# Kernel optimization log

Hardware: AMD Instinct MI355X
Metric: run time of the kernel (lower is better)

The kernel has to match this reference:

```python
import jax, jax.numpy as jnp
import numpy as np

D_MODEL = 256
LATENT = 64
OBJ = 32
OUT_DIM = LATENT + OBJ  # 96
STEPS = 50
BETA_START = 1e-4
BETA_END = 0.02
LN_EPS = 1e-5


def _gru_layer(x, w_ih, w_hh, b_ih, b_hh):
    # x: [B, T, din]; weights in torch layout: [3*d, din], [3*d, d]
    B = x.shape[0]
    d = w_hh.shape[1]

    def step(h, xt):
        gi = xt @ w_ih.T + b_ih
        gh = h @ w_hh.T + b_hh
        i_r, i_z, i_n = jnp.split(gi, 3, axis=-1)
        h_r, h_z, h_n = jnp.split(gh, 3, axis=-1)
        r = jax.nn.sigmoid(i_r + h_r)
        z = jax.nn.sigmoid(i_z + h_z)
        n = jnp.tanh(i_n + r * h_n)
        h_new = (1.0 - z) * n + z * h
        return h_new, h_new

    h0 = jnp.zeros((B, d), x.dtype)
    _, ys = jax.lax.scan(step, h0, jnp.swapaxes(x, 0, 1))
    return jnp.swapaxes(ys, 0, 1)


def setup_inputs() -> dict:
    key = jax.random.key(0)
    ks = jax.random.split(key, 24)
    B, T = 8, 512
    D, IN = D_MODEL, OUT_DIM
    s = 0.02
    inp = {
        "z_seq": jax.random.normal(ks[0], (B, T, LATENT), jnp.float32),
        "o_seq": jax.random.normal(ks[1], (B, T, OBJ), jnp.float32),
        "in_proj_w": jax.random.normal(ks[2], (D, IN), jnp.float32) * s,
        "in_proj_b": jnp.zeros((D,), jnp.float32),
        "gru_wih0": jax.random.normal(ks[3], (3 * D, D), jnp.float32) * s,
        "gru_whh0": jax.random.normal(ks[4], (3 * D, D), jnp.float32) * s,
        "gru_bih0": jnp.zeros((3 * D,), jnp.float32),
        "gru_bhh0": jnp.zeros((3 * D,), jnp.float32),
        "gru_wih1": jax.random.normal(ks[5], (3 * D, D), jnp.float32) * s,
        "gru_whh1": jax.random.normal(ks[6], (3 * D, D), jnp.float32) * s,
        "gru_bih1": jnp.zeros((3 * D,), jnp.float32),
        "gru_bhh1": jnp.zeros((3 * D,), jnp.float32),
        "ln_g": jnp.ones((D,), jnp.float32),
        "ln_b": jnp.zeros((D,), jnp.float32),
        "time_w1": jax.random.normal(ks[7], (D, 1), jnp.float32) * s,
        "time_b1": jnp.zeros((D,), jnp.float32),
        "time_w2": jax.random.normal(ks[8], (D, D), jnp.float32) * s,
        "time_b2": jnp.zeros((D,), jnp.float32),
        "den_w1": jax.random.normal(ks[9], (2 * D, OUT_DIM + 2 * D), jnp.float32) * s,
        "den_b1": jnp.zeros((2 * D,), jnp.float32),
        "den_w2": jax.random.normal(ks[10], (2 * D, 2 * D), jnp.float32) * s,
        "den_b2": jnp.zeros((2 * D,), jnp.float32),
        "den_w3": jax.random.normal(ks[11], (OUT_DIM, 2 * D), jnp.float32) * s,
        "den_b3": jnp.zeros((OUT_DIM,), jnp.float32),
    }
    return inp


def _forward(z_seq, o_seq, in_proj_w, in_proj_b, gru_wih0, gru_whh0, gru_bih0,
             gru_bhh0, gru_wih1, gru_whh1, gru_bih1, gru_bhh1, ln_g, ln_b,
             time_w1, time_b1, time_w2, time_b2, den_w1, den_b1, den_w2,
             den_b2, den_w3, den_b3):
    # --- conditioning: concat -> in_proj -> 2-layer GRU -> LayerNorm
    x = jnp.concatenate([z_seq, o_seq], axis=-1)            # [B,T,in_dim]
    hcond = x @ in_proj_w.T + in_proj_b                     # [B,T,D]
    hcond = _gru_layer(hcond, gru_wih0, gru_whh0, gru_bih0, gru_bhh0)
    hcond = _gru_layer(hcond, gru_wih1, gru_whh1, gru_bih1, gru_bhh1)
    mu = jnp.mean(hcond, axis=-1, keepdims=True)
    var = jnp.mean(jnp.square(hcond - mu), axis=-1, keepdims=True)
    hcond = (hcond - mu) * jax.lax.rsqrt(var + LN_EPS) * ln_g + ln_b

    B, T, _ = hcond.shape

    # --- diffusion schedule buffers
    betas = jnp.linspace(BETA_START, BETA_END, STEPS, dtype=jnp.float32)
    alphas = 1.0 - betas
    alpha_bars = jnp.cumprod(alphas)
    sqrt_recip_alphas = jnp.sqrt(1.0 / alphas)

    noise_key = jax.random.key(42)
    x0 = jax.random.normal(jax.random.fold_in(noise_key, STEPS),
                           (B, T, OUT_DIM), jnp.float32)

    def body(x_t, step):
        # time embedding: t_norm is a scalar (same for every token), broadcast
        t_norm = step.astype(jnp.float32) / float(max(1, STEPS - 1))
        e = jax.nn.silu(t_norm * time_w1[:, 0] + time_b1)   # [D]
        t_emb = e @ time_w2.T + time_b2                     # [D]
        t_emb = jnp.broadcast_to(t_emb, (B, T, D_MODEL))

        inp = jnp.concatenate([x_t, hcond, t_emb], axis=-1)  # [B,T,96+2D]
        y = jax.nn.silu(inp @ den_w1.T + den_b1)
        y = jax.nn.silu(y @ den_w2.T + den_b2)
        eps_theta = y @ den_w3.T + den_b3                   # [B,T,96]

        beta_t = betas[step]
        coeff = beta_t / jnp.sqrt(1.0 - alpha_bars[step])
        mean = sqrt_recip_alphas[step] * (x_t - coeff * eps_theta)
        noise = jax.random.normal(jax.random.fold_in(noise_key, step),
                                  x_t.shape, x_t.dtype)
        x_next = jnp.where(step > 0, mean + jnp.sqrt(beta_t) * noise, mean)
        return x_next, None

    steps = jnp.arange(STEPS - 1, -1, -1)
    x_t, _ = jax.lax.scan(body, x0, steps)
    return x_t


def reference(z_seq, o_seq, in_proj_w, in_proj_b, gru_wih0, gru_whh0, gru_bih0,
              gru_bhh0, gru_wih1, gru_whh1, gru_bih1, gru_bhh1, ln_g, ln_b,
              time_w1, time_b1, time_w2, time_b2, den_w1, den_b1, den_w2,
              den_b2, den_w3, den_b3):
    x_t = _forward(z_seq, o_seq, in_proj_w, in_proj_b, gru_wih0, gru_whh0,
                   gru_bih0, gru_bhh0, gru_wih1, gru_whh1, gru_bih1, gru_bhh1,
                   ln_g, ln_b, time_w1, time_b1, time_w2, time_b2, den_w1,
                   den_b1, den_w2, den_b2, den_w3, den_b3)
    return x_t[..., :LATENT], x_t[..., LATENT:]
```

## Files before the change

### kernel.cpp

```cpp
#include <hip/hip_runtime.h>
#include <stdint.h>
#include <math.h>

#define DM    256
#define G3    768
#define TT    512
#define BB    8
#define MM    4096
#define OUTD  96
#define HH2   512
#define NSTEPS 50
#define NTOT  (MM*OUTD)
#define NZTOT ((NSTEPS+1)*NTOT)
#define CH    16
#define NCH   (TT/CH)
#define F0 0
#define F1 8
#define F2 16
#define F3 24
#define FW1 32

typedef _Float16 f16;
typedef _Float16 f16x2 __attribute__((ext_vector_type(2)));
typedef _Float16 f16x8 __attribute__((ext_vector_type(8)));
typedef float    f32x4 __attribute__((ext_vector_type(4)));

__device__ __forceinline__ void lds_barrier() {
  asm volatile("s_waitcnt lgkmcnt(0)" ::: "memory");
  __builtin_amdgcn_s_barrier();
}

__device__ __forceinline__ void wait_flag(const uint32_t* f, uint32_t target) {
  if (threadIdx.x == 0) {
    while (__hip_atomic_load(f, __ATOMIC_RELAXED, __HIP_MEMORY_SCOPE_AGENT) < target)
      __builtin_amdgcn_s_sleep(8);
  }
  __builtin_amdgcn_s_barrier();
  __builtin_amdgcn_fence(__ATOMIC_ACQUIRE, "agent");
}

__host__ __device__ inline void tf2x32(uint32_t k0, uint32_t k1,
                                       uint32_t x0, uint32_t x1,
                                       uint32_t& o0, uint32_t& o1)
{
  uint32_t ks2 = k0 ^ k1 ^ 0x1BD11BDAu;
#define ROTL(v,r) (((v)<<(r))|((v)>>(32-(r))))
#define RND(r) { x0 += x1; x1 = ROTL(x1,r); x1 ^= x0; }
  x0 += k0; x1 += k1;
  RND(13) RND(15) RND(26) RND(6)
  x0 += k1;  x1 += ks2 + 1u;
  RND(17) RND(29) RND(16) RND(24)
  x0 += ks2; x1 += k0 + 2u;
  RND(13) RND(15) RND(26) RND(6)
  x0 += k0;  x1 += k1 + 3u;
  RND(17) RND(29) RND(16) RND(24)
  x0 += k1;  x1 += ks2 + 4u;
  RND(13) RND(15) RND(26) RND(6)
  x0 += ks2; x1 += k0 + 5u;
  o0 = x0; o1 = x1;
#undef RND
#undef ROTL
}

__device__ inline float bits_to_normal(uint32_t bits) {
  float f = __uint_as_float((bits >> 9) | 0x3F800000u) - 1.0f;
  const float lo = -0.99999994f;
  float u = fmaxf(lo, f * 2.0f + lo);
  float w = -log1pf(-u * u);
  float p;
  if (w < 5.0f) {
    w -= 2.5f;
    p = 2.81022636e-08f;
    p = fmaf(p, w, 3.43273939e-07f);
    p = fmaf(p, w, -3.5233877e-06f);
    p = fmaf(p, w, -4.39150654e-06f);
    p = fmaf(p, w, 0.00021858087f);
    p = fmaf(p, w, -0.00125372503f);
    p = fmaf(p, w, -0.00417768164f);
    p = fmaf(p, w, 0.246640727f);
    p = fmaf(p, w, 1.50140941f);
  } else {
    w = sqrtf(w) - 3.0f;
    p = -0.000200214257f;
    p = fmaf(p, w, 0.000100950558f);
    p = fmaf(p, w, 0.00134934322f);
    p = fmaf(p, w, -0.00367342844f);
    p = fmaf(p, w, 0.00573950773f);
    p = fmaf(p, w, -0.0076224613f);
    p = fmaf(p, w, 0.00943887047f);
    p = fmaf(p, w, 1.00167406f);
    p = fmaf(p, w, 2.83297682f);
  }
  float ei = p * u;
  return 1.41421356f * ei;
}

__device__ inline float jax_normal_elem(uint32_t k0, uint32_t k1, uint32_t e) {
  uint32_t o0, o1;
  tf2x32(k0, k1, 0u, e, o0, o1);
  return bits_to_normal(o0 ^ o1);
}

__device__ inline float dot2f(f16x2 a, f16x2 b, float c) {
#if __has_builtin(__builtin_amdgcn_fdot2)
  return __builtin_amdgcn_fdot2(a, b, c, false);
#else
  return c + (float)a[0]*(float)b[0] + (float)a[1]*(float)b[1];
#endif
}
__device__ inline float sigmoidf_(float x) { return 1.f / (1.f + __expf(-x)); }
__device__ inline float siluf_(float x)    { return x / (1.f + __expf(-x)); }
__device__ inline float tanhf_(float x) {
  float e = __expf(-2.f * fabsf(x));
  float t = (1.f - e) / (1.f + e);
  return copysignf(t, x);
}

__device__ inline unsigned char f32_to_e4m3(float f) {
#if __has_builtin(__builtin_amdgcn_cvt_pk_fp8_f32)
  int p = __builtin_amdgcn_cvt_pk_fp8_f32(f, f, 0, false);
  return (unsigned char)(p & 0xff);
#else
  uint32_t u = __float_as_uint(f);
  unsigned char s = (unsigned char)((u >> 24) & 0x80);
  float af = fabsf(f);
  if (!(af == af)) return (unsigned char)(s | 0x7f);
  if (af >= 448.f) return (unsigned char)(s | 0x7e);
  if (af < 0.0078125f) {
    int q = (int)rintf(af * 512.f);
    return (unsigned char)(s | q);
  }
  int e; float m = frexpf(af, &e);
  int mant = (int)rintf(m * 16.f);
  if (mant == 16) { mant = 8; e += 1; }
  int E = e - 1 + 7;
  if (E <= 0) { int q = (int)rintf(af * 512.f); return (unsigned char)(s | q); }
  return (unsigned char)(s | (E << 3) | (mant - 8));
#endif
}

struct DiffParams {
  float sra[NSTEPS], coeff[NSTEPS], sb[NSTEPS];
  uint32_t k0[NSTEPS], k1[NSTEPS];
  uint32_t xk0, xk1;
};

template<bool WF, bool WH, bool PUB, bool WAIT>
__device__ __forceinline__ void scan_body(int b, int d,
    const float* __restrict__ gi, const f16* __restrict__ whh,
    const float* __restrict__ bhh,
    float* __restrict__ hf_out, f16* __restrict__ hh_out,
    f16 (*hbuf)[128], uint32_t* pubf, const uint32_t* waitf)
{
  f16x8 wr[16], wz[16], wn[16];
  {
    const f16x8* pr = (const f16x8*)(whh + (size_t)d*DM);
    const f16x8* pz = (const f16x8*)(whh + (size_t)(256+d)*DM);
    const f16x8* pn = (const f16x8*)(whh + (size_t)(512+d)*DM);
    #pragma unroll
    for (int q = 0; q < 16; q++) { wr[q]=pr[q]; wz[q]=pz[q]; wn[q]=pn[q]; }
  }
  if (d < 128) { hbuf[0][d] = (f16)0.f; hbuf[1][d] = (f16)0.f; }
  const float bn = bhh[512 + d];
  float h_old = 0.f;
  __syncthreads();
  const size_t rowbase = (size_t)b * TT;
  if (WAIT) wait_flag(waitf, 2u * 2u);
  float gr[4], gz[4], gn[4];
  #pragma unroll
  for (int i = 0; i < 3; i++) {
    const float* gp = gi + (rowbase + i)*G3;
    gr[i] = gp[d]; gz[i] = gp[256+d]; gn[i] = gp[512+d];
  }
  #pragma unroll 4
  for (int t = 0; t < TT; t++) {
    if (WAIT && t && (t & (CH-1)) == 0) {
      int c = t / CH;
      int nc = c + 2 > NCH ? NCH : c + 2;
      wait_flag(waitf, 2u * (uint32_t)nc);
    }
    const int sl = t & 3;
    const int sl3 = (t + 3) & 3;
    if (t + 3 < TT) {
      const float* gp = gi + (rowbase + t + 3)*G3;
      gr[sl3] = gp[d]; gz[sl3] = gp[256+d]; gn[sl3] = gp[512+d];
    }
    float ar0=0.f, ar1=0.f, az0=0.f, az1=0.f, an0=0.f, an1=0.f;
    const f16x8* hb = (const f16x8*)hbuf[t & 1];
    #pragma unroll
    for (int q = 0; q < 16; q++) {
      f16x8 hv = hb[q];
      f16x8 w0 = wr[q], w1 = wz[q], w2 = wn[q];
      #pragma unroll
      for (int pp = 0; pp < 4; pp++) {
        f16x2 ha; ha[0]=hv[2*pp]; ha[1]=hv[2*pp+1];
        f16x2 vr; vr[0]=w0[2*pp]; vr[1]=w0[2*pp+1];
        f16x2 vz; vz[0]=w1[2*pp]; vz[1]=w1[2*pp+1];
        f16x2 vn; vn[0]=w2[2*pp]; vn[1]=w2[2*pp+1];
        if (pp & 1) { ar1=dot2f(ha,vr,ar1); az1=dot2f(ha,vz,az1); an1=dot2f(ha,vn,an1); }
        else        { ar0=dot2f(ha,vr,ar0); az0=dot2f(ha,vz,az0); an0=dot2f(ha,vn,an0); }
      }
    }
    float rr = sigmoidf_((ar0+ar1) + gr[sl]);
    float zz = sigmoidf_((az0+az1) + gz[sl]);
    float nv = tanhf_(gn[sl] + rr * ((an0+an1) + bn));
    float hn = (1.f - zz) * nv + zz * h_old;
    h_old = hn;
    if (d < 128) hbuf[(t & 1) ^ 1][d] = (f16)hn;
    size_t o = (rowbase + t)*DM + d;
    if (WF) hf_out[o] = hn;
    if (WH) hh_out[o] = (f16)hn;
    if (PUB && ((t + 1) & (CH-1)) == 0) {
      __syncthreads();
      if (d == 0)
        __hip_atomic_store(pubf, (uint32_t)(t + 1), __ATOMIC_RELEASE,
                           __HIP_MEMORY_SCOPE_AGENT);
    } else {
      lds_barrier();
    }
  }
}

__device__ __forceinline__ void gi_gemm_chunks(int b, int nh, int t,
    const f16* __restrict__ A, const f16* __restrict__ Bw,
    const float* __restrict__ bias, float* __restrict__ Y,
    const uint32_t* waitf, uint32_t* pubf)
{
  const int lane = t & 63, wave = t >> 6;
  const int n0w = nh*384 + wave*96;
  const int l15 = lane & 15, quad = lane >> 4;
  const int kq = quad*8, rb = quad*4;
  for (int c = 0; c < NCH; c++) {
    if (waitf) wait_flag(waitf, (uint32_t)((c+1)*CH));
    const f16* Ap = A + ((size_t)b*TT + c*CH + l15)*DM + kq;
    f32x4 acc[6] = {};
    #pragma unroll
    for (int kt = 0; kt < 8; kt++) {
      f16x8 a = *(const f16x8*)(Ap + kt*32);
      #pragma unroll
      for (int nt = 0; nt < 6; nt++) {
        const f16* Bp = Bw + (size_t)(n0w + nt*16 + l15)*DM + kq + kt*32;
        acc[nt] = __builtin_amdgcn_mfma_f32_16x16x32_f16(a, *(const f16x8*)Bp, acc[nt], 0,0,0);
      }
    }
    #pragma unroll
    for (int nt = 0; nt < 6; nt++) {
      int n = n0w + nt*16 + l15;
      float bb = bias[n];
      #pragma unroll
      for (int r = 0; r < 4; r++)
        Y[((size_t)b*TT + c*CH + rb + r)*G3 + n] = acc[nt][r] + bb;
    }
    __syncthreads();
    if (t == 0)
      __hip_atomic_fetch_add(pubf, 1u, __ATOMIC_RELEASE, __HIP_MEMORY_SCOPE_AGENT);
  }
}

__global__ __launch_bounds__(256)
void k_inproj_mega(const float* __restrict__ z, const float* __restrict__ o,
                   const float* __restrict__ W, const float* __restrict__ b,
                   f16* __restrict__ hh,
                   const float* __restrict__ wih0, f16* __restrict__ wih0h,
                   const float* __restrict__ whh0, f16* __restrict__ whh0h,
                   const float* __restrict__ bih0, const float* __restrict__ bhh0,
                   float* __restrict__ cb0,
                   const float* __restrict__ wih1, f16* __restrict__ wih1h,
                   const float* __restrict__ whh1, f16* __restrict__ whh1h,
                   const float* __restrict__ bih1, const float* __restrict__ bhh1,
                   float* __restrict__ cb1, uint32_t* __restrict__ flags)
{
  const int blk = blockIdx.x, d = threadIdx.x;
  __shared__ float xs[96];
  if (blk < MM) {
    const int m = blk;
    if (d < 64) xs[d] = z[m*64 + d];
    else if (d < 96) xs[d] = o[m*32 + d - 64];
    __syncthreads();
    const float* wr = W + d*96;
    float acc = b[d];
    #pragma unroll
    for (int k = 0; k < 96; k++) acc = fmaf(xs[k], wr[k], acc);
    hh[m*DM + d] = (f16)acc;
  } else if (blk < MM + 96) {
    for (int i = (blk - MM)*256 + d; i < G3*DM; i += 96*256) wih0h[i] = (f16)wih0[i];
  } else if (blk < MM + 192) {
    for (int i = (blk - MM - 96)*256 + d; i < G3*DM; i += 96*256) whh0h[i] = (f16)whh0[i];
  } else if (blk == MM + 192) {
    for (int j = d; j < G3; j += 256) cb0[j] = bih0[j] + (j < 512 ? bhh0[j] : 0.f);
  } else if (blk < MM + 289) {
    for (int i = (blk - MM - 193)*256 + d; i < G3*DM; i += 96*256) wih1h[i] = (f16)wih1[i];
  } else if (blk < MM + 385) {
    for (int i = (blk - MM - 289)*256 + d; i < G3*DM; i += 96*256) whh1h[i] = (f16)whh1[i];
  } else if (blk == MM + 385) {
    for (int j = d; j < G3; j += 256) cb1[j] = bih1[j] + (j < 512 ? bhh1[j] : 0.f);
  } else {
    if (d < 33) flags[d] = 0u;
  }
}

__global__ __launch_bounds__(256, 1)
void k_scan_pipe(float* __restrict__ gi,
                 const f16* __restrict__ whh0h, const float* __restrict__ bhh0,
                 f16* __restrict__ h0h,
                 const f16* __restrict__ wih0h, const float* __restrict__ cb0,
                 const f16* __restrict__ wih1h, const float* __restrict__ cb1,
                 const f16* __restrict__ whh1h, const float* __restrict__ bhh1,
                 float* __restrict__ hA,
                 const float* __restrict__ ln_g, const float* __restrict__ ln_b,
                 const f16* __restrict__ w1hh, f16* __restrict__ hpreh,
                 uint32_t* __restrict__ flags,
                 const float* __restrict__ dw2, unsigned char* __restrict__ w2p,
                 const float* __restrict__ dw3, f16* __restrict__ w3h,
                 const float* __restrict__ dw1, f16* __restrict__ w1x,
                 f16* __restrict__ w1h,
                 const float* __restrict__ tw1, const float* __restrict__ tb1,
                 const float* __restrict__ tw2, const float* __restrict__ tb2,
                 const float* __restrict__ db1, float* __restrict__ tv,
                 f16* __restrict__ nzb, DiffParams P)
{
  __shared__ f16 hbuf[2][128];
  __shared__ float e[DM], te[DM];
  __shared__ f16 hc[16][264];
  const int blk = blockIdx.x, t = threadIdx.x;
  if (blk < 16) {
    const int b = blk >> 1, nh = blk & 1;
    gi_gemm_chunks(b, nh, t, h0h, wih0h, cb0, gi, nullptr, &flags[F3 + b]);
  } else if (blk < 24) {
    const int b = blk - 16;
    scan_body<false, true, true, true>(b, t, gi, whh0h, bhh0,
                                       nullptr, h0h, hbuf,
                                       &flags[F0 + b], &flags[F3 + b]);
  } else if (blk < 40) {
    const int g = blk - 24, b = g >> 1, nh = g & 1;
    gi_gemm_chunks(b, nh, t, h0h, wih1h, cb1, gi, &flags[F0 + b], &flags[F1 + b]);
  } else if (blk < 48) {
    const int b = blk - 40;
    scan_body<true, false, true, true>(b, t, gi, whh1h, bhh1,
                                       hA, nullptr, hbuf,
                                       &flags[F2 + b], &flags[F1 + b]);
  } else if (blk < 112) {
    for (int i = (blk - 48)*256 + t; i < 512*512; i += 64*256) {
      int j = i & 7;
      int lane = (i >> 3) & 63;
      int tk = i >> 9;
      int tt = tk >> 4, kt = tk & 15;
      int row = tt*16 + (lane & 15);
      int col = kt*32 + (lane >> 4)*8 + j;
      w2p[i] = f32_to_e4m3(dw2[row*512 + col]);
    }
  } else if (blk < 128) {
    for (int i = (blk - 112)*256 + t; i < OUTD*HH2; i += 16*256) w3h[i] = (f16)dw3[i];
  } else if (blk < 184) {
    for (int i = (blk - 128)*256 + t; i < 512*96 + 512*256; i += 56*256) {
      if (i < 512*96) { int n = i/96, k = i%96; w1x[i] = (f16)dw1[n*608 + k]; }
      else { int jj = i - 512*96; int n = jj/256, k = jj%256; w1h[jj] = (f16)dw1[n*608 + 96 + k]; }
    }
    __syncthreads();
    if (t == 0)
      __hip_atomic_fetch_add(&flags[FW1], 1u, __ATOMIC_RELEASE, __HIP_MEMORY_SCOPE_AGENT);
  } else if (blk < 234) {
    const int s = blk - 184;
    float tn = (float)s / 49.f;
    { float v = tn * tw1[t] + tb1[t]; e[t] = siluf_(v); }
    __syncthreads();
    {
      float acc = tb2[t];
      const float* wr = tw2 + t*DM;
      #pragma unroll 8
      for (int k = 0; k < DM; k++) acc = fmaf(e[k], wr[k], acc);
      te[t] = acc;
    }
    __syncthreads();
    for (int n = t; n < HH2; n += 256) {
      float a2 = db1[n];
      const float* r = dw1 + n*608 + 352;
      #pragma unroll 8
      for (int k = 0; k < DM; k++) a2 = fmaf(te[k], r[k], a2);
      tv[s*HH2 + n] = a2;
    }
  } else if (blk < 298) {
    const int g = blk - 234, b = g >> 3, cg = g & 7;
    wait_flag(&flags[FW1], 56u);
    const int wave = t >> 6, lane = t & 63;
    float gl0=ln_g[lane], gl1=ln_g[lane+64], gl2=ln_g[lane+128], gl3=ln_g[lane+192];
    float bl0=ln_b[lane], bl1=ln_b[lane+64], bl2=ln_b[lane+128], bl3=ln_b[lane+192];
    for (int k4 = 0; k4 < 4; k4++) {
      const int c = cg*4 + k4;
      wait_flag(&flags[F2 + b], (uint32_t)((c+1)*CH));
      const size_t R0 = (size_t)b*TT + c*CH;
      #pragma unroll
      for (int rr = 0; rr < 4; rr++) {
        int r = wave*4 + rr;
        const float* row = hA + (R0 + r)*DM;
        float v0=row[lane], v1=row[lane+64], v2=row[lane+128], v3=row[lane+192];
        float s = v0+v1+v2+v3;
        #pragma unroll
        for (int o2 = 32; o2; o2 >>= 1) s += __shfl_xor(s, o2, 64);
        float mu = s * (1.f/256.f);
        float d0=v0-mu, d1=v1-mu, d2=v2-mu, d3=v3-mu;
        float q = d0*d0+d1*d1+d2*d2+d3*d3;
        #pragma unroll
        for (int o2 = 32; o2; o2 >>= 1) q += __shfl_xor(q, o2, 64);
        float rs = rsqrtf(q*(1.f/256.f) + 1e-5f);
        hc[r][lane]     = (f16)(d0*rs*gl0 + bl0);
        hc[r][lane+64]  = (f16)(d1*rs*gl1 + bl1);
        hc[r][lane+128] = (f16)(d2*rs*gl2 + bl2);
        hc[r][lane+192] = (f16)(d3*rs*gl3 + bl3);
      }
      __syncthreads();
      const int l15 = lane & 15, quad = lane >> 4;
      const int kq = quad*8, rb = quad*4;
      f32x4 acc[8] = {};
      #pragma unroll
      for (int kt = 0; kt < 8; kt++) {
        f16x8 a = *(const f16x8*)&hc[l15][kt*32 + kq];
        #pragma unroll
        for (int nt = 0; nt < 8; nt++) {
          const f16* Bp = w1hh + (size_t)(wave*128 + nt*16 + l15)*DM + kq + kt*32;
          acc[nt] = __builtin_amdgcn_mfma_f32_16x16x32_f16(a, *(const f16x8*)Bp, acc[nt], 0,0,0);
        }
      }
      #pragma unroll
      for (int nt = 0; nt < 8; nt++) {
        int n = wave*128 + nt*16 + l15;
        #pragma unroll
        for (int r = 0; r < 4; r++)
          hpreh[(R0 + rb + r)*HH2 + n] = (f16)acc[nt][r];
      }
      __syncthreads();
    }
  } else {
    long base = (long)(blk - 298) * 9792;
    long end  = base + 9792;
    while (base < end) {
      int s = (int)(base / NTOT);
      long segend = (long)(s + 1) * NTOT;
      if (segend > end) segend = end;
      uint32_t kk0 = (s < NSTEPS) ? P.k0[s] : P.xk0;
      uint32_t kk1 = (s < NSTEPS) ? P.k1[s] : P.xk1;
      long sbase = (long)s * NTOT;
      for (long ee = base + t; ee < segend; ee += 256)
        nzb[ee] = (f16)jax_normal_elem(kk0, kk1, (uint32_t)(ee - sbase));
      base = segend;
    }
  }
}

#define YSTR  520
#define XHSTR 104
#define W3STR 520

__device__ __forceinline__ int y1p_swz(int g) {
  return ((g >> 2) & 7) | ((g & 3) << 3) | (g & 32);
}

__global__ __launch_bounds__(1024)
void k_diff(const f16* __restrict__ w1x,
            const unsigned char* __restrict__ w2p,
            const f16* __restrict__ w3h,
            const f16* __restrict__ hpreh,
            const float* __restrict__ tv,
            const float* __restrict__ db2,
            const float* __restrict__ db3,
            const f16* __restrict__ nzb,
            float* __restrict__ out,
            DiffParams P)
{
  __shared__ unsigned char y1p_l[16*512];
  __shared__ f16 y2_l[16*YSTR];
  __shared__ f16 xh_l[16*XHSTR];
  __shared__ f16 w3_l[96*W3STR];

  const int t = threadIdx.x;
  const int lane = t & 63;
  const int wave = t >> 6;
  const int quad = lane >> 4;
  const int l15 = lane & 15;
  const int m0 = blockIdx.x * 16;
  const int n0w = wave * 32;

  const int t0 = 2*wave, t1 = 2*wave + 1;
  const int lsw8 = y1p_swz(lane) << 3;

  long w2f0[16], w2f1[16];
  {
    const unsigned char* p0 = w2p + (((size_t)(t0*16)*64 + lane) << 3);
    const unsigned char* p1 = w2p + (((size_t)(t1*16)*64 + lane) << 3);
    #pragma unroll
    for (int kt = 0; kt < 16; kt++) {
      w2f0[kt] = *(const long*)(p0 + kt*512);
      w2f1[kt] = *(const long*)(p1 + kt*512);
    }
  }
  float hpr[2][4];
  #pragma unroll
  for (int nt = 0; nt < 2; nt++)
    #pragma unroll
    for (int r = 0; r < 4; r++)
      hpr[nt][r] = (float)hpreh[(long)(m0 + quad*4 + r)*HH2 + n0w + nt*16 + l15];
  const float db2r0 = db2[n0w + l15];
  const float db2r1 = db2[n0w + 16 + l15];

  #pragma unroll
  for (int i = 0; i < 6; i++) {
    int v = t + i*1024;
    int row = v >> 6, c8 = v & 63;
    *((f16x8*)&w3_l[row*W3STR] + c8) = *((const f16x8*)(w3h + row*HH2) + c8);
  }

  const int neps = wave * 16 + l15;
  float xreg[4];
  if (wave < 6) {
    #pragma unroll
    for (int r = 0; r < 4; r++) {
      int ml = quad*4 + r;
      float v = (float)nzb[(size_t)NSTEPS*NTOT + (size_t)(m0 + ml)*OUTD + neps];
      xreg[r] = v;
      xh_l[ml*XHSTR + neps] = (f16)v;
    }
  }

  for (int s = NSTEPS-1; s >= 0; --s) {
    __syncthreads();
    f16 nzr[4];
    if (wave < 6 && s > 0) {
      #pragma unroll
      for (int r = 0; r < 4; r++)
        nzr[r] = nzb[(size_t)s*NTOT + (size_t)(m0 + quad*4 + r)*OUTD + neps];
    }
    {
      f32x4 acc[2] = {};
      #pragma unroll
      for (int kt = 0; kt < 3; kt++) {
        f16x8 a = *(const f16x8*)&xh_l[l15*XHSTR + kt*32 + quad*8];
        f16x8 b0 = *(const f16x8*)&w1x[(n0w + l15)*96 + kt*32 + quad*8];
        f16x8 b1 = *(const f16x8*)&w1x[(n0w + 16 + l15)*96 + kt*32 + quad*8];
        acc[0] = __builtin_amdgcn_mfma_f32_16x16x32_f16(a, b0, acc[0], 0,0,0);
        acc[1] = __builtin_amdgcn_mfma_f32_16x16x32_f16(a, b1, acc[1], 0,0,0);
      }
      #pragma unroll
      for (int nt = 0; nt < 2; nt++) {
        int n = n0w + nt*16 + l15;
        float tvv = tv[s*HH2 + n];
        int lp = ((nt*2 + (l15>>3)) << 4);
        int jp = l15 & 7;
        #pragma unroll
        for (int r = 0; r < 4; r++) {
          float v = (nt ? acc[1][r] : acc[0][r]) + hpr[nt][r] + tvv;
          int ml = quad*4 + r;
          y1p_l[wave*512 + (y1p_swz(ml | lp) << 3) + jp] = f32_to_e4m3(siluf_(v));
        }
      }
    }
    lds_barrier();
    {
      f32x4 acc2[2] = {};
      #pragma unroll
      for (int kt = 0; kt < 16; kt++) {
        long a  = *(const long*)(y1p_l + kt*512 + lsw8);
        acc2[0] = __builtin_amdgcn_mfma_f32_16x16x32_fp8_fp8(a, w2f0[kt], acc2[0], 0,0,0);
        acc2[1] = __builtin_amdgcn_mfma_f32_16x16x32_fp8_fp8(a, w2f1[kt], acc2[1], 0,0,0);
      }
      #pragma unroll
      for (int nt = 0; nt < 2; nt++) {
        int n = n0w + nt*16 + l15;
        float bb = nt ? db2r1 : db2r0;
        #pragma unroll
        for (int r = 0; r < 4; r++) {
          int ml = quad*4 + r;
          y2_l[ml*YSTR + n] = (f16)siluf_((nt ? acc2[1][r] : acc2[0][r]) + bb);
        }
      }
    }
    lds_barrier();
    if (wave < 6) {
      f32x4 acc3 = {};
      #pragma unroll 8
      for (int kt = 0; kt < 16; kt++) {
        f16x8 a = *(const f16x8*)&y2_l[l15*YSTR + kt*32 + quad*8];
        f16x8 b = *(const f16x8*)&w3_l[(wave*16 + l15)*W3STR + kt*32 + quad*8];
        acc3 = __builtin_amdgcn_mfma_f32_16x16x32_f16(a, b, acc3, 0,0,0);
      }
      float sra = P.sra[s], coeff = P.coeff[s], sb = P.sb[s];
      float b3 = db3[neps];
      #pragma unroll
      for (int r = 0; r < 4; r++) {
        int ml = quad*4 + r;
        float eps = acc3[r] + b3;
        float mean = sra * (xreg[r] - coeff * eps);
        float xn = mean;
        if (s > 0) xn = mean + sb * (float)nzr[r];
        xreg[r] = xn;
        xh_l[ml*XHSTR + neps] = (f16)xn;
      }
    }
  }
  if (wave < 6) {
    #pragma unroll
    for (int r = 0; r < 4; r++) {
      long m = m0 + quad*4 + r;
      if (neps < 64) out[m*64 + neps] = xreg[r];
      else out[(long)MM*64 + m*32 + (neps - 64)] = xreg[r];
    }
  }
}

extern "C" void kernel_launch(void* const* d_in, const int* in_sizes, int n_in,
                              void* d_out, int out_size, void* d_ws, size_t ws_size,
                              hipStream_t stream)
{
  (void)in_sizes; (void)n_in; (void)out_size; (void)ws_size;
  const float* z_seq = (const float*)d_in[0];
  const float* o_seq = (const float*)d_in[1];
  const float* in_w  = (const float*)d_in[2];
  const float* in_b  = (const float*)d_in[3];
  const float* wih0  = (const float*)d_in[4];
  const float* whh0  = (const float*)d_in[5];
  const float* bih0  = (const float*)d_in[6];
  const float* bhh0  = (const float*)d_in[7];
  const float* wih1  = (const float*)d_in[8];
  const float* whh1  = (const float*)d_in[9];
  const float* bih1  = (const float*)d_in[10];
  const float* bhh1  = (const float*)d_in[11];
  const float* ln_g  = (const float*)d_in[12];
  const float* ln_b  = (const float*)d_in[13];
  const float* tw1   = (const float*)d_in[14];
  const float* tb1   = (const float*)d_in[15];
  const float* tw2   = (const float*)d_in[16];
  const float* tb2   = (const float*)d_in[17];
  const float* dw1   = (const float*)d_in[18];
  const float* db1   = (const float*)d_in[19];
  const float* dw2   = (const float*)d_in[20];
  const float* db2   = (const float*)d_in[21];
  const float* dw3   = (const float*)d_in[22];
  const float* db3   = (const float*)d_in[23];

  char* base = (char*)d_ws;
  size_t off = 0;
  auto alloc = [&](size_t bytes) -> void* {
    void* p = base + off;
    off = (off + bytes + 255) & ~(size_t)255;
    return p;
  };
  float* gi     = (float*)alloc((size_t)MM*G3*4);
  float* hA     = (float*)alloc((size_t)MM*DM*4);
  f16*   hAh    = (f16*)  alloc((size_t)MM*DM*2);
  f16*   hpreh  = (f16*)  alloc((size_t)MM*HH2*2);
  float* tv     = (float*)alloc((size_t)NSTEPS*HH2*4);
  f16*   wih0h  = (f16*)  alloc((size_t)G3*DM*2);
  f16*   whh0h  = (f16*)  alloc((size_t)G3*DM*2);
  f16*   wih1h  = (f16*)  alloc((size_t)G3*DM*2);
  f16*   whh1h  = (f16*)  alloc((size_t)G3*DM*2);
  f16*   w1xh   = (f16*)  alloc((size_t)HH2*96*2);
  f16*   w1hh   = (f16*)  alloc((size_t)HH2*DM*2);
  unsigned char* w2p = (unsigned char*)alloc((size_t)HH2*HH2);
  f16*   w3h    = (f16*)  alloc((size_t)OUTD*HH2*2);
  float* cb0    = (float*)alloc((size_t)G3*4);
  float* cb1    = (float*)alloc((size_t)G3*4);
  uint32_t* flags = (uint32_t*)alloc(256);
  f16*   nzb    = (f16*)  alloc((size_t)NZTOT*2);

  DiffParams P;
  {
    float ab = 1.f;
    float delta = (0.02f - 1e-4f) / 49.f;
    for (int i = 0; i < NSTEPS; i++) {
      float bt = 1e-4f + delta * (float)i;
      float al = 1.f - bt;
      ab *= al;
      P.sra[i]   = sqrtf(1.f / al);
      P.coeff[i] = bt / sqrtf(1.f - ab);
      P.sb[i]    = sqrtf(bt);
    }
    for (int s = 0; s < NSTEPS; s++) {
      uint32_t o0, o1;
      tf2x32(0u, 42u, 0u, (uint32_t)s, o0, o1);
      P.k0[s] = o0; P.k1[s] = o1;
    }
    uint32_t o0, o1;
    tf2x32(0u, 42u, 0u, (uint32_t)NSTEPS, o0, o1);
    P.xk0 = o0; P.xk1 = o1;
  }

  k_inproj_mega<<<MM + 387, 256, 0, stream>>>(
      z_seq, o_seq, in_w, in_b, hAh,
      wih0, wih0h, whh0, whh0h, bih0, bhh0, cb0,
      wih1, wih1h, whh1, whh1h, bih1, bhh1, cb1, flags);
  k_scan_pipe<<<298 + 2048, 256, 0, stream>>>(
      gi, whh0h, bhh0, hAh, wih0h, cb0,
      wih1h, cb1, whh1h, bhh1, hA,
      ln_g, ln_b, w1hh, hpreh, flags,
      dw2, w2p, dw3, w3h, dw1, w1xh, w1hh,
      tw1, tb1, tw2, tb2, db1, tv, nzb, P);
  k_diff<<<256, 1024, 0, stream>>>(w1xh, w2p, w3h, hpreh, tv, db2, db3, nzb,
                                   (float*)d_out, P);
}
```

Baseline: 845.3 us.

## Fold input projection into GRU layer-0 input weights and bias

Precomputes Wc = W_ih0 · W_in (768×96) and the matching combined bias, so layer-0 gate inputs come straight from the concatenated 96-wide inputs. This drops the separate per-row input-projection pass (4096 blocks) and the W_ih0 fp16 conversion. It also cuts the layer-0 input GEMM depth from 256 to 96 by templating the chunked GEMM on K. The cost is a small weight-product prep step and slightly different rounding, since the product is stored in fp16.

```diff
diff --git a/kernel.cpp b/kernel.cpp
--- a/kernel.cpp
+++ b/kernel.cpp
@@ -221,25 +221,27 @@
   }
 }
 
+template<int KT>
 __device__ __forceinline__ void gi_gemm_chunks(int b, int nh, int t,
     const f16* __restrict__ A, const f16* __restrict__ Bw,
     const float* __restrict__ bias, float* __restrict__ Y,
     const uint32_t* waitf, uint32_t* pubf)
 {
+  const int K = KT * 32;
   const int lane = t & 63, wave = t >> 6;
   const int n0w = nh*384 + wave*96;
   const int l15 = lane & 15, quad = lane >> 4;
   const int kq = quad*8, rb = quad*4;
   for (int c = 0; c < NCH; c++) {
     if (waitf) wait_flag(waitf, (uint32_t)((c+1)*CH));
-    const f16* Ap = A + ((size_t)b*TT + c*CH + l15)*DM + kq;
+    const f16* Ap = A + ((size_t)b*TT + c*CH + l15)*K + kq;
     f32x4 acc[6] = {};
     #pragma unroll
-    for (int kt = 0; kt < 8; kt++) {
+    for (int kt = 0; kt < KT; kt++) {
       f16x8 a = *(const f16x8*)(Ap + kt*32);
       #pragma unroll
       for (int nt = 0; nt < 6; nt++) {
-        const f16* Bp = Bw + (size_t)(n0w + nt*16 + l15)*DM + kq + kt*32;
+        const f16* Bp = Bw + (size_t)(n0w + nt*16 + l15)*K + kq + kt*32;
         acc[nt] = __builtin_amdgcn_mfma_f32_16x16x32_f16(a, *(const f16x8*)Bp, acc[nt], 0,0,0);
       }
     }
@@ -258,44 +260,49 @@
 }
 
 __global__ __launch_bounds__(256)
-void k_inproj_mega(const float* __restrict__ z, const float* __restrict__ o,
-                   const float* __restrict__ W, const float* __restrict__ b,
-                   f16* __restrict__ hh,
-                   const float* __restrict__ wih0, f16* __restrict__ wih0h,
-                   const float* __restrict__ whh0, f16* __restrict__ whh0h,
-                   const float* __restrict__ bih0, const float* __restrict__ bhh0,
-                   float* __restrict__ cb0,
-                   const float* __restrict__ wih1, f16* __restrict__ wih1h,
-                   const float* __restrict__ whh1, f16* __restrict__ whh1h,
-                   const float* __restrict__ bih1, const float* __restrict__ bhh1,
-                   float* __restrict__ cb1, uint32_t* __restrict__ flags)
+void k_prep(const float* __restrict__ z, const float* __restrict__ o,
+            const float* __restrict__ in_w, const float* __restrict__ in_b,
+            const float* __restrict__ wih0, const float* __restrict__ whh0,
+            f16* __restrict__ whh0h,
+            const float* __restrict__ bih0, const float* __restrict__ bhh0,
+            const float* __restrict__ wih1, f16* __restrict__ wih1h,
+            const float* __restrict__ whh1, f16* __restrict__ whh1h,
+            const float* __restrict__ bih1, const float* __restrict__ bhh1,
+            float* __restrict__ cb1,
+            f16* __restrict__ xh96, f16* __restrict__ Wc, float* __restrict__ cbc,
+            uint32_t* __restrict__ flags)
 {
-  const int blk = blockIdx.x, d = threadIdx.x;
-  __shared__ float xs[96];
-  if (blk < MM) {
-    const int m = blk;
-    if (d < 64) xs[d] = z[m*64 + d];
-    else if (d < 96) xs[d] = o[m*32 + d - 64];
-    __syncthreads();
-    const float* wr = W + d*96;
-    float acc = b[d];
-    #pragma unroll
-    for (int k = 0; k < 96; k++) acc = fmaf(xs[k], wr[k], acc);
-    hh[m*DM + d] = (f16)acc;
-  } else if (blk < MM + 96) {
-    for (int i = (blk - MM)*256 + d; i < G3*DM; i += 96*256) wih0h[i] = (f16)wih0[i];
-  } else if (blk < MM + 192) {
-    for (int i = (blk - MM - 96)*256 + d; i < G3*DM; i += 96*256) whh0h[i] = (f16)whh0[i];
-  } else if (blk == MM + 192) {
-    for (int j = d; j < G3; j += 256) cb0[j] = bih0[j] + (j < 512 ? bhh0[j] : 0.f);
-  } else if (blk < MM + 289) {
-    for (int i = (blk - MM - 193)*256 + d; i < G3*DM; i += 96*256) wih1h[i] = (f16)wih1[i];
-  } else if (blk < MM + 385) {
-    for (int i = (blk - MM - 289)*256 + d; i < G3*DM; i += 96*256) whh1h[i] = (f16)whh1[i];
-  } else if (blk == MM + 385) {
-    for (int j = d; j < G3; j += 256) cb1[j] = bih1[j] + (j < 512 ? bhh1[j] : 0.f);
+  const int blk = blockIdx.x, t = threadIdx.x;
+  if (blk < 96) {
+    for (int i = blk*256 + t; i < G3*DM; i += 96*256) whh0h[i] = (f16)whh0[i];
+  } else if (blk < 192) {
+    for (int i = (blk-96)*256 + t; i < G3*DM; i += 96*256) wih1h[i] = (f16)wih1[i];
+  } else if (blk < 288) {
+    for (int i = (blk-192)*256 + t; i < G3*DM; i += 96*256) whh1h[i] = (f16)whh1[i];
+  } else if (blk < 384) {
+    for (int i = (blk-288)*256 + t; i < MM*OUTD; i += 96*256) {
+      int row = i / OUTD, c = i % OUTD;
+      float v = (c < 64) ? z[row*64 + c] : o[row*32 + c - 64];
+      xh96[i] = (f16)v;
+    }
+  } else if (blk < 672) {
+    int idx = (blk-384)*256 + t;
+    int n = idx / OUTD, k = idx % OUTD;
+    const float* wr = wih0 + (size_t)n*DM;
+    float acc = 0.f;
+    #pragma unroll 8
+    for (int d = 0; d < DM; d++) acc = fmaf(wr[d], in_w[d*OUTD + k], acc);
+    Wc[idx] = (f16)acc;
+  } else if (blk < 675) {
+    int j = (blk-672)*256 + t;
+    const float* wr = wih0 + (size_t)j*DM;
+    float acc = bih0[j] + (j < 512 ? bhh0[j] : 0.f);
+    #pragma unroll 8
+    for (int d = 0; d < DM; d++) acc = fmaf(wr[d], in_b[d], acc);
+    cbc[j] = acc;
   } else {
-    if (d < 33) flags[d] = 0u;
+    for (int j = t; j < G3; j += 256) cb1[j] = bih1[j] + (j < 512 ? bhh1[j] : 0.f);
+    if (t < 33) flags[t] = 0u;
   }
 }
 
@@ -303,7 +310,8 @@
 void k_scan_pipe(float* __restrict__ gi,
                  const f16* __restrict__ whh0h, const float* __restrict__ bhh0,
                  f16* __restrict__ h0h,
-                 const f16* __restrict__ wih0h, const float* __restrict__ cb0,
+                 const f16* __restrict__ xh96, const f16* __restrict__ Wc,
+                 const float* __restrict__ cbc,
                  const f16* __restrict__ wih1h, const float* __restrict__ cb1,
                  const f16* __restrict__ whh1h, const float* __restrict__ bhh1,
                  float* __restrict__ hA,
@@ -325,7 +333,7 @@
   const int blk = blockIdx.x, t = threadIdx.x;
   if (blk < 16) {
     const int b = blk >> 1, nh = blk & 1;
-    gi_gemm_chunks(b, nh, t, h0h, wih0h, cb0, gi, nullptr, &flags[F3 + b]);
+    gi_gemm_chunks<3>(b, nh, t, xh96, Wc, cbc, gi, nullptr, &flags[F3 + b]);
   } else if (blk < 24) {
     const int b = blk - 16;
     scan_body<false, true, true, true>(b, t, gi, whh0h, bhh0,
@@ -333,7 +341,7 @@
                                        &flags[F0 + b], &flags[F3 + b]);
   } else if (blk < 40) {
     const int g = blk - 24, b = g >> 1, nh = g & 1;
-    gi_gemm_chunks(b, nh, t, h0h, wih1h, cb1, gi, &flags[F0 + b], &flags[F1 + b]);
+    gi_gemm_chunks<8>(b, nh, t, h0h, wih1h, cb1, gi, &flags[F0 + b], &flags[F1 + b]);
   } else if (blk < 48) {
     const int b = blk - 40;
     scan_body<true, false, true, true>(b, t, gi, whh1h, bhh1,
@@ -648,7 +656,6 @@
   f16*   hAh    = (f16*)  alloc((size_t)MM*DM*2);
   f16*   hpreh  = (f16*)  alloc((size_t)MM*HH2*2);
   float* tv     = (float*)alloc((size_t)NSTEPS*HH2*4);
-  f16*   wih0h  = (f16*)  alloc((size_t)G3*DM*2);
   f16*   whh0h  = (f16*)  alloc((size_t)G3*DM*2);
   f16*   wih1h  = (f16*)  alloc((size_t)G3*DM*2);
   f16*   whh1h  = (f16*)  alloc((size_t)G3*DM*2);
@@ -656,7 +663,9 @@
   f16*   w1hh   = (f16*)  alloc((size_t)HH2*DM*2);
   unsigned char* w2p = (unsigned char*)alloc((size_t)HH2*HH2);
   f16*   w3h    = (f16*)  alloc((size_t)OUTD*HH2*2);
-  float* cb0    = (float*)alloc((size_t)G3*4);
+  f16*   xh96   = (f16*)  alloc((size_t)MM*OUTD*2);
+  f16*   Wc     = (f16*)  alloc((size_t)G3*OUTD*2);
+  float* cbc    = (float*)alloc((size_t)G3*4);
   float* cb1    = (float*)alloc((size_t)G3*4);
   uint32_t* flags = (uint32_t*)alloc(256);
   f16*   nzb    = (f16*)  alloc((size_t)NZTOT*2);
@@ -683,12 +692,13 @@
     P.xk0 = o0; P.xk1 = o1;
   }
 
-  k_inproj_mega<<<MM + 387, 256, 0, stream>>>(
-      z_seq, o_seq, in_w, in_b, hAh,
-      wih0, wih0h, whh0, whh0h, bih0, bhh0, cb0,
-      wih1, wih1h, whh1, whh1h, bih1, bhh1, cb1, flags);
+  k_prep<<<676, 256, 0, stream>>>(
+      z_seq, o_seq, in_w, in_b,
+      wih0, whh0, whh0h, bih0, bhh0,
+      wih1, wih1h, whh1, whh1h, bih1, bhh1, cb1,
+      xh96, Wc, cbc, flags);
   k_scan_pipe<<<298 + 2048, 256, 0, stream>>>(
-      gi, whh0h, bhh0, hAh, wih0h, cb0,
+      gi, whh0h, bhh0, hAh, xh96, Wc, cbc,
       wih1h, cb1, whh1h, bhh1, hA,
       ln_g, ln_b, w1hh, hpreh, flags,
       dw2, w2p, dw3, w3h, dw1, w1xh, w1hh,
```

New measurement: 812.2 us (median of 2 runs). 1.04x faster.
